# Kernel tuning notes

Hardware: AMD Instinct MI355X
Metric: run time of the kernel (lower is better)

Reference implementation:

```python
import jax, jax.numpy as jnp
import numpy as np

E, H, F = 8, 2048, 1024  # num_experts, hidden_size, moe_intermediate_size
T = 8192                 # tokens


def setup_inputs() -> dict:
    key = jax.random.key(0)
    ks = jax.random.split(key, 6)
    hidden_states = jax.random.normal(ks[0], (T, H), dtype=jnp.float32)
    routing_weights = jax.random.uniform(ks[1], (T, 2), dtype=jnp.float32)
    selected_experts = jax.random.randint(ks[2], (T, 2), 0, E)
    # torch nn.Linear weight layout: [out_features, in_features]
    scale_h = 1.0 / np.sqrt(H)
    scale_f = 1.0 / np.sqrt(F)
    gate_w = jax.random.normal(ks[3], (E, F, H), dtype=jnp.float32) * scale_h
    up_w = jax.random.normal(ks[4], (E, F, H), dtype=jnp.float32) * scale_h
    down_w = jax.random.normal(ks[5], (E, H, F), dtype=jnp.float32) * scale_f
    return {
        "hidden_states": hidden_states,
        "routing_weights": routing_weights,
        "selected_experts": selected_experts,
        "gate_w": gate_w,
        "up_w": up_w,
        "down_w": down_w,
    }


def reference(hidden_states, routing_weights, selected_experts, gate_w, up_w, down_w):
    # routing_weights / selected_experts are accepted but unused: uniform 1/E routing.
    uniform_weight = 1.0 / gate_w.shape[0]
    final_hidden = jnp.zeros_like(hidden_states)
    for e in range(gate_w.shape[0]):  # small fixed expert count
        gate = jax.nn.gelu(hidden_states @ gate_w[e].T, approximate=True)  # [T, F]
        up = hidden_states @ up_w[e].T                                     # [T, F]
        final_hidden = final_hidden + (gate * up) @ down_w[e].T * uniform_weight
    return final_hidden
```

## Files before the change

kernel.cpp:

```cpp
#include <hip/hip_runtime.h>
#include <stdint.h>

#define TT  8192
#define HD  2048
#define FD  1024
#define NE  8
#define EFD 8192

typedef short bf16x8 __attribute__((ext_vector_type(8)));
typedef float f32x4  __attribute__((ext_vector_type(4)));
typedef unsigned short u16;

__device__ __forceinline__ u16 f2bf(float x) {
  union { float f; uint32_t u; } v; v.f = x;
  uint32_t r = v.u + 0x7fffu + ((v.u >> 16) & 1u);
  return (u16)(r >> 16);
}

__device__ __forceinline__ float gelu_tanh(float x) {
  float y = 0.7978845608028654f * (x + 0.044715f * x * x * x);
  float e = __expf(2.0f * y);
  return x - x / (e + 1.0f);
}

__device__ __forceinline__ void gload_lds16(const u16* g, const u16* lds_uniform) {
  __builtin_amdgcn_global_load_lds(
      (__attribute__((address_space(1))) void*)(uintptr_t)g,
      (__attribute__((address_space(3))) void*)(uint32_t)(uintptr_t)lds_uniform,
      16, 0, 0);
}

__global__ __launch_bounds__(256) void k_cast_x(const float* __restrict__ s,
                                                u16* __restrict__ d) {
  long i = ((long)blockIdx.x * 256 + threadIdx.x) * 8;
  float4 a = *(const float4*)(s + i);
  float4 b = *(const float4*)(s + i + 4);
  *(ushort4*)(d + i)     = make_ushort4(f2bf(a.x), f2bf(a.y), f2bf(a.z), f2bf(a.w));
  *(ushort4*)(d + i + 4) = make_ushort4(f2bf(b.x), f2bf(b.y), f2bf(b.z), f2bf(b.w));
}

__global__ __launch_bounds__(256) void k_cast_w(const float* __restrict__ gw,
                                                const float* __restrict__ uw,
                                                u16* __restrict__ wb) {
  const int f = blockIdx.x, e = blockIdx.y, s = blockIdx.z;
  const float* src = (s ? uw : gw) + ((long)e * FD + f) * HD + threadIdx.x * 8;
  const int n = ((f >> 4) << 5) + (s << 4) + (f & 15);
  u16* d = wb + ((long)e * 2 * FD + n) * HD + threadIdx.x * 8;
  float4 a = ((const float4*)src)[0];
  float4 b = ((const float4*)src)[1];
  *(ushort4*)(d)     = make_ushort4(f2bf(a.x), f2bf(a.y), f2bf(a.z), f2bf(a.w));
  *(ushort4*)(d + 4) = make_ushort4(f2bf(b.x), f2bf(b.y), f2bf(b.z), f2bf(b.w));
}

__global__ __launch_bounds__(256) void k_cast_down(const float* __restrict__ dw,
                                                   u16* __restrict__ b2) {
  int e   = blockIdx.y;
  int idx = blockIdx.x * 256 + threadIdx.x;
  int h   = idx >> 7;
  int fc  = idx & 127;
  const float* s = dw + (long)e * HD * FD + (long)h * FD + fc * 8;
  float4 a = ((const float4*)s)[0];
  float4 b = ((const float4*)s)[1];
  u16* d = b2 + (long)h * EFD + e * FD + fc * 8;
  *(ushort4*)(d)     = make_ushort4(f2bf(a.x), f2bf(a.y), f2bf(a.z), f2bf(a.w));
  *(ushort4*)(d + 4) = make_ushort4(f2bf(b.x), f2bf(b.y), f2bf(b.z), f2bf(b.w));
}

template<int NKT, int LDA, int LDB>
__device__ __forceinline__ void gemm_core(const u16* __restrict__ Ag,
                                          const u16* __restrict__ Bg,
                                          f32x4 (&acc)[8][4]) {
  __shared__ __align__(16) u16 Al[2 * 2 * 16 * 512];
  __shared__ __align__(16) u16 Bl[2 * 2 * 16 * 512];

  const int t    = threadIdx.x;
  const int lane = t & 63;
  const int w    = t >> 6;
  const int wm   = w >> 2;
  const int wn   = w & 3;
  const int r4   = lane >> 2;
  const int gch  = ((lane & 3) - ((lane >> 3) & 3)) & 3;
  const int rb0  = w * 2, rb1 = rb0 + 1;

  const u16* A0 = Ag + (long)(rb0 * 16 + r4) * LDA + gch * 8;
  const u16* A1 = Ag + (long)(rb1 * 16 + r4) * LDA + gch * 8;
  const u16* B0 = Bg + (long)(rb0 * 16 + r4) * LDB + gch * 8;
  const u16* B1 = Bg + (long)(rb1 * 16 + r4) * LDB + gch * 8;

  u16* const Ad0 = Al + rb0 * 512;
  u16* const Ad1 = Al + rb1 * 512;
  u16* const Bd0 = Bl + rb0 * 512;
  u16* const Bd1 = Bl + rb1 * 512;

  const int q = lane >> 4, c = lane & 15;
  const int coff = c * 32 + (((q + (c >> 1)) & 3) * 8);

  bf16x8 af[8], bf0, bf1;

#define STAGE_A(buf, ks, kt) do {                                              \
    gload_lds16(A0 + (kt) * 64 + (ks) * 32, Ad0 + (buf) * 16384 + (ks) * 8192); \
    gload_lds16(A1 + (kt) * 64 + (ks) * 32, Ad1 + (buf) * 16384 + (ks) * 8192); \
  } while (0)
#define STAGE_B(buf, ks, kt) do {                                              \
    gload_lds16(B0 + (kt) * 64 + (ks) * 32, Bd0 + (buf) * 16384 + (ks) * 8192); \
    gload_lds16(B1 + (kt) * 64 + (ks) * 32, Bd1 + (buf) * 16384 + (ks) * 8192); \
  } while (0)
#define LD_AF(buf, ks) do { _Pragma("unroll")                                  \
    for (int i = 0; i < 8; ++i)                                                \
      af[i] = *(const bf16x8*)(Al + (buf) * 16384 + (ks) * 8192 +              \
                               (wm * 8 + i) * 512 + coff);                     \
  } while (0)
#define LD_BF(buf, ks, jh) do {                                                \
    bf0 = *(const bf16x8*)(Bl + (buf) * 16384 + (ks) * 8192 +                  \
                           (wn * 4 + (jh) * 2 + 0) * 512 + coff);              \
    bf1 = *(const bf16x8*)(Bl + (buf) * 16384 + (ks) * 8192 +                  \
                           (wn * 4 + (jh) * 2 + 1) * 512 + coff);              \
  } while (0)
#define MFMA_HALF(jh) do { _Pragma("unroll")                                   \
    for (int i = 0; i < 8; ++i) {                                              \
      acc[i][(jh) * 2 + 0] = __builtin_amdgcn_mfma_f32_16x16x32_bf16(          \
          af[i], bf0, acc[i][(jh) * 2 + 0], 0, 0, 0);                          \
      acc[i][(jh) * 2 + 1] = __builtin_amdgcn_mfma_f32_16x16x32_bf16(          \
          af[i], bf1, acc[i][(jh) * 2 + 1], 0, 0, 0);                          \
    } } while (0)
#define BAR   __builtin_amdgcn_s_barrier()
#define LGKM0 do { asm volatile("s_waitcnt lgkmcnt(0)" ::: "memory");          \
                   __builtin_amdgcn_sched_barrier(0); } while (0)
#define VM(n) asm volatile("s_waitcnt vmcnt(" #n ")" ::: "memory")

  STAGE_A(0, 0, 0); STAGE_B(0, 0, 0);
  STAGE_A(0, 1, 0); STAGE_B(0, 1, 0);
  STAGE_A(1, 0, 1); STAGE_B(1, 0, 1);
  VM(8); BAR;

#define PHASE(buf, ks, jh, STG, DOVM) do {                                     \
    if ((jh) == 0) LD_AF(buf, ks);                                             \
    LD_BF(buf, ks, jh);                                                        \
    STG;                                                                       \
    BAR; LGKM0;                                                                \
    __builtin_amdgcn_s_setprio(1);                                             \
    MFMA_HALF(jh);                                                             \
    __builtin_amdgcn_s_setprio(0);                                             \
    if (DOVM) VM(8);                                                           \
    BAR;                                                                       \
  } while (0)

#define KTILE(kt, buf) do {                                                    \
    const int kn1 = ((kt) + 1) & (NKT - 1);                                    \
    const int kn2 = ((kt) + 2) & (NKT - 1);                                    \
    PHASE(buf, 0, 0, STAGE_A((buf) ^ 1, 1, kn1), 0);                           \
    PHASE(buf, 0, 1, STAGE_B((buf) ^ 1, 1, kn1), 1);                           \
    PHASE(buf, 1, 0, STAGE_A((buf), 0, kn2), 0);                               \
    PHASE(buf, 1, 1, STAGE_B((buf), 0, kn2), 1);                               \
  } while (0)

  for (int kt = 0; kt < NKT; kt += 2) {
    KTILE(kt, 0);
    KTILE(kt + 1, 1);
  }
  VM(0);

#undef KTILE
#undef PHASE
#undef VM
#undef LGKM0
#undef BAR
#undef MFMA_HALF
#undef LD_BF
#undef LD_AF
#undef STAGE_B
#undef STAGE_A
}

__global__ __launch_bounds__(512, 2) void k_gemm1(const u16* __restrict__ Xb,
                                                  const u16* __restrict__ Wb,
                                                  u16* __restrict__ In) {
  const int bid = blockIdx.x;
  const int s   = (bid & 7) * 256 + (bid >> 3);
  const int e   = s >> 8;
  const int rem = s & 255;
  const int m0  = (rem >> 3) * 256;
  const int n0  = (rem & 7) * 256;

  f32x4 acc[8][4] = {};
  gemm_core<HD / 64, HD, HD>(Xb + (long)m0 * HD,
                             Wb + ((long)e * 2 * FD + n0) * HD, acc);

  const int t = threadIdx.x, lane = t & 63, w = t >> 6;
  const int wm = w >> 2, wn = w & 3;
  const int q = lane >> 4, c = lane & 15;
#pragma unroll
  for (int i = 0; i < 8; ++i)
#pragma unroll
    for (int jj = 0; jj < 2; ++jj) {
      const int  mr  = m0 + wm * 128 + i * 16 + q * 4;
      const long col = (long)e * FD + (n0 >> 1) + wn * 32 + jj * 16 + c;
#pragma unroll
      for (int r = 0; r < 4; ++r) {
        float g = acc[i][2 * jj + 0][r];
        float u = acc[i][2 * jj + 1][r];
        In[(long)(mr + r) * EFD + col] = f2bf(gelu_tanh(g) * u);
      }
    }
}

__global__ __launch_bounds__(512, 2) void k_gemm2(const u16* __restrict__ In,
                                                  const u16* __restrict__ Db,
                                                  float* __restrict__ out) {
  const int bid = blockIdx.x;
  const int s   = (bid & 7) * 32 + (bid >> 3);
  const int m0  = (s >> 3) * 256;
  const int n0  = (s & 7) * 256;

  f32x4 acc[8][4] = {};
  gemm_core<EFD / 64, EFD, EFD>(In + (long)m0 * EFD, Db + (long)n0 * EFD, acc);

  const int t = threadIdx.x, lane = t & 63, w = t >> 6;
  const int wm = w >> 2, wn = w & 3;
  const int q = lane >> 4, c = lane & 15;
#pragma unroll
  for (int i = 0; i < 8; ++i)
#pragma unroll
    for (int j = 0; j < 4; ++j) {
      const int mr = m0 + wm * 128 + i * 16 + q * 4;
      const int nc = n0 + wn * 64 + j * 16 + c;
#pragma unroll
      for (int r = 0; r < 4; ++r)
        out[(long)(mr + r) * HD + nc] = acc[i][j][r] * 0.125f;
    }
}

extern "C" void kernel_launch(void* const* d_in, const int* in_sizes, int n_in,
                              void* d_out, int out_size, void* d_ws, size_t ws_size,
                              hipStream_t stream) {
  const float* X  = (const float*)d_in[0];
  const float* gw = (const float*)d_in[3];
  const float* uw = (const float*)d_in[4];
  const float* dw = (const float*)d_in[5];
  float* out = (float*)d_out;

  char* ws = (char*)d_ws;
  u16* Xb = (u16*)(ws);
  u16* Wb = (u16*)(ws + (size_t)32  * 1024 * 1024);
  u16* Db = (u16*)(ws + (size_t)96  * 1024 * 1024);
  u16* In = (u16*)(ws + (size_t)128 * 1024 * 1024);

  k_cast_x<<<dim3(8192), 256, 0, stream>>>(X, Xb);
  k_cast_w<<<dim3(FD, NE, 2), 256, 0, stream>>>(gw, uw, Wb);
  k_cast_down<<<dim3(1024, NE), 256, 0, stream>>>(dw, Db);

  k_gemm1<<<dim3(2048), 512, 0, stream>>>(Xb, Wb, In);
  k_gemm2<<<dim3(256), 512, 0, stream>>>(In, Db, out);
}
```

Before: 937.5 us.

## Software-pipeline LDS fragment loads ahead of MFMA phases in GEMM mainloop

Restructures the GEMM main loop so the LDS register-fragment loads for the next phase are issued right after the current MFMA batch, before the barrier. The explicit lgkmcnt(0) wait before the MFMAs is removed, so LDS reads overlap with the global-to-LDS staging and barrier waits. The vmcnt threshold is lowered from 8 to 4 and sched_barriers pin the instruction order. This relies on compiler-inserted waitcnts for correctness and changes how much global-load latency hiding the loop has.

```diff
diff --git a/kernel.cpp b/kernel.cpp
--- a/kernel.cpp
+++ b/kernel.cpp
@@ -124,34 +124,39 @@
           af[i], bf1, acc[i][(jh) * 2 + 1], 0, 0, 0);                          \
     } } while (0)
 #define BAR   __builtin_amdgcn_s_barrier()
-#define LGKM0 do { asm volatile("s_waitcnt lgkmcnt(0)" ::: "memory");          \
-                   __builtin_amdgcn_sched_barrier(0); } while (0)
+#define SB0   __builtin_amdgcn_sched_barrier(0)
 #define VM(n) asm volatile("s_waitcnt vmcnt(" #n ")" ::: "memory")
+#define PRIO1 __builtin_amdgcn_s_setprio(1)
+#define PRIO0 __builtin_amdgcn_s_setprio(0)
 
   STAGE_A(0, 0, 0); STAGE_B(0, 0, 0);
   STAGE_A(0, 1, 0); STAGE_B(0, 1, 0);
   STAGE_A(1, 0, 1); STAGE_B(1, 0, 1);
-  VM(8); BAR;
-
-#define PHASE(buf, ks, jh, STG, DOVM) do {                                     \
-    if ((jh) == 0) LD_AF(buf, ks);                                             \
-    LD_BF(buf, ks, jh);                                                        \
-    STG;                                                                       \
-    BAR; LGKM0;                                                                \
-    __builtin_amdgcn_s_setprio(1);                                             \
-    MFMA_HALF(jh);                                                             \
-    __builtin_amdgcn_s_setprio(0);                                             \
-    if (DOVM) VM(8);                                                           \
-    BAR;                                                                       \
-  } while (0)
+  VM(4); SB0; BAR;
+  LD_BF(0, 0, 0); LD_AF(0, 0);
+  SB0;
 
 #define KTILE(kt, buf) do {                                                    \
     const int kn1 = ((kt) + 1) & (NKT - 1);                                    \
     const int kn2 = ((kt) + 2) & (NKT - 1);                                    \
-    PHASE(buf, 0, 0, STAGE_A((buf) ^ 1, 1, kn1), 0);                           \
-    PHASE(buf, 0, 1, STAGE_B((buf) ^ 1, 1, kn1), 1);                           \
-    PHASE(buf, 1, 0, STAGE_A((buf), 0, kn2), 0);                               \
-    PHASE(buf, 1, 1, STAGE_B((buf), 0, kn2), 1);                               \
+                  \
+    STAGE_A((buf) ^ 1, 1, kn1); SB0; BAR;                                      \
+    PRIO1; MFMA_HALF(0); PRIO0;                                                \
+    LD_BF(buf, 0, 1); SB0; BAR;                                                \
+           \
+    STAGE_B((buf) ^ 1, 1, kn1); SB0; BAR;                                      \
+    PRIO1; MFMA_HALF(1); PRIO0;                                                \
+    VM(4);                                                                     \
+    LD_BF(buf, 1, 0); LD_AF(buf, 1); SB0; BAR;                                 \
+                  \
+    STAGE_A(buf, 0, kn2); SB0; BAR;                                            \
+    PRIO1; MFMA_HALF(0); PRIO0;                                                \
+    LD_BF(buf, 1, 1); SB0; BAR;                                                \
+    \
+    STAGE_B(buf, 0, kn2); SB0; BAR;                                            \
+    PRIO1; MFMA_HALF(1); PRIO0;                                                \
+    VM(4);                                                                     \
+    LD_BF((buf) ^ 1, 0, 0); LD_AF((buf) ^ 1, 0); SB0; BAR;                     \
   } while (0)
 
   for (int kt = 0; kt < NKT; kt += 2) {
@@ -161,9 +166,10 @@
   VM(0);
 
 #undef KTILE
-#undef PHASE
+#undef PRIO0
+#undef PRIO1
 #undef VM
-#undef LGKM0
+#undef SB0
 #undef BAR
 #undef MFMA_HALF
 #undef LD_BF
```

New measurement: 949.4 us. No clear change (+1.3%).
